# Kernel tuning notes

Measured on AMD Instinct MI355X. Metric: run time of the kernel, lower is better.

Reference implementation:

```python
import jax, jax.numpy as jnp
import numpy as np

D_MODEL = 1024
H = 16
D_K = D_MODEL // H
B, S = 2, 2048


def setup_inputs() -> dict:
    key = jax.random.key(0)
    ks = jax.random.split(key, 11)
    sc = 1.0 / np.sqrt(D_MODEL)
    inp = {
        "q": jax.random.normal(ks[0], (B, S, D_MODEL), jnp.float32),
        "k": jax.random.normal(ks[1], (B, S, D_MODEL), jnp.float32),
        "v": jax.random.normal(ks[2], (B, S, D_MODEL), jnp.float32),
        "mask": jnp.ones((1, 1, S, S), dtype=bool),
        # nn.Linear weights are [out, in]; y = x @ W.T + b
        "wq_w": jax.random.normal(ks[3], (D_MODEL, D_MODEL), jnp.float32) * sc,
        "wq_b": jnp.zeros((D_MODEL,), jnp.float32),
        "wk_w": jax.random.normal(ks[4], (D_MODEL, D_MODEL), jnp.float32) * sc,
        "wk_b": jnp.zeros((D_MODEL,), jnp.float32),
        "wv_w": jax.random.normal(ks[5], (D_MODEL, D_MODEL), jnp.float32) * sc,
        "wv_b": jnp.zeros((D_MODEL,), jnp.float32),
        "wo_w": jax.random.normal(ks[6], (D_MODEL, D_MODEL), jnp.float32) * sc,
        "wo_b": jnp.zeros((D_MODEL,), jnp.float32),
    }
    return inp


def _split_heads(x):
    b, s, _ = x.shape
    return x.reshape(b, s, H, D_K).transpose(0, 2, 1, 3)  # [B,H,S,Dk]


def reference(q, k, v, mask, wq_w, wq_b, wk_w, wk_b, wv_w, wv_b, wo_w, wo_b):
    # projections (nn.Linear: x @ W.T + b)
    qh = _split_heads(q @ wq_w.T + wq_b)
    kh = _split_heads(k @ wk_w.T + wk_b)
    vh = _split_heads(v @ wv_w.T + wv_b)
    # scaled dot-product attention with additive -1e9 masking
    scores = jnp.einsum("bhqd,bhkd->bhqk", qh, kh) / jnp.sqrt(jnp.float32(D_K))
    scores = jnp.where(mask, scores, jnp.float32(-1e9))
    attn = jax.nn.softmax(scores, axis=-1)  # dropout p=0.0 -> identity
    out = jnp.einsum("bhqk,bhkd->bhqd", attn, vh)
    out = out.transpose(0, 2, 1, 3).reshape(q.shape[0], q.shape[1], D_MODEL)
    return out @ wo_w.T + wo_b
```

## Files before the change

kernel.cpp:

```cpp
#include <hip/hip_runtime.h>
#include <hip/hip_bf16.h>


typedef unsigned short u16;
typedef unsigned int u32;
typedef short s16x4 __attribute__((ext_vector_type(4)));
typedef short s16x8 __attribute__((ext_vector_type(8)));
typedef float f32x4 __attribute__((ext_vector_type(4)));

#define NH 16

__device__ __forceinline__ u16 f2bf(float f) {
  u32 u = __builtin_bit_cast(u32, f);
  u32 r = (u + 0x7fffu + ((u >> 16) & 1u)) >> 16;
  return (u16)r;
}

__device__ __forceinline__ void stage16(const void* g, void* l) {
  __builtin_amdgcn_global_load_lds((const __attribute__((address_space(1))) void*)g,
                                   (__attribute__((address_space(3))) void*)l,
                                   16, 0, 0);
}

__global__ __launch_bounds__(256) void convert3(const float* __restrict__ a,
                                                const float* __restrict__ b,
                                                const float* __restrict__ c,
                                                u16* da, u16* db, u16* dc) {
  const float* s = blockIdx.y == 0 ? a : (blockIdx.y == 1 ? b : c);
  u16* d = blockIdx.y == 0 ? da : (blockIdx.y == 1 ? db : dc);
  int i = (blockIdx.x * 256 + threadIdx.x) * 4;
  f32x4 v = *(const f32x4*)(s + i);
  s16x4 o;
#pragma unroll
  for (int j = 0; j < 4; ++j) o[j] = (short)f2bf(v[j]);
  *(s16x4*)(d + i) = o;
}

__global__ __launch_bounds__(256) void convert4(const float* __restrict__ a,
                                                const float* __restrict__ b,
                                                const float* __restrict__ c,
                                                const float* __restrict__ e,
                                                u16* da, u16* db, u16* dc, u16* de) {
  const float* s = blockIdx.y == 0 ? a
                   : (blockIdx.y == 1 ? b : (blockIdx.y == 2 ? c : e));
  u16* d = blockIdx.y == 0 ? da : (blockIdx.y == 1 ? db : (blockIdx.y == 2 ? dc : de));
  int i = (blockIdx.x * 256 + threadIdx.x) * 4;
  f32x4 v = *(const f32x4*)(s + i);
  s16x4 o;
#pragma unroll
  for (int j = 0; j < 4; ++j) o[j] = (short)f2bf(v[j]);
  *(s16x4*)(d + i) = o;
}

#define GEMM_CORE(A_, W_)                                                      \
  const int tid = threadIdx.x;                                                 \
  const int lane = tid & 63;                                                   \
  const int wid = tid >> 6;                                                    \
  const int l16 = lane & 15, quad = lane >> 4;                                 \
  const int wm = (wid >> 1) * 64, wn = (wid & 1) * 64;                         \
  const int m0 = blockIdx.y * 128;                                             \
  const int n0 = blockIdx.x * 128;                                             \
  const int ra = tid >> 2;                                                     \
  const int c8 = (tid & 3) ^ (ra & 3);                                         \
  const u16* Abase = A_ + (size_t)(m0 + ra) * 1024 + c8 * 8;                   \
  const u16* A2 = Abase + (size_t)64 * 1024;                                   \
  const u16* Wbase = W_ + (size_t)(n0 + ra) * 1024 + c8 * 8;                   \
  const u16* W2 = Wbase + (size_t)64 * 1024;                                   \
  u16* ldsA = As + tid * 8;                                                    \
  u16* ldsB = Bs + tid * 8;                                                    \
  f32x4 acc[4][4];                                                             \
  _Pragma("unroll") for (int i = 0; i < 4; ++i)                                \
  _Pragma("unroll") for (int j = 0; j < 4; ++j)                                \
      acc[i][j] = (f32x4){0.f, 0.f, 0.f, 0.f};                                 \
  for (int k0 = 0; k0 < 1024; k0 += 32) {                                      \
    __syncthreads();                                                           \
    stage16(Abase + k0, ldsA);                                                 \
    stage16(A2 + k0, ldsA + 2048);                                             \
    stage16(Wbase + k0, ldsB);                                                 \
    stage16(W2 + k0, ldsB + 2048);                                             \
    __syncthreads();                                                           \
    s16x8 bfr[4];                                                              \
    _Pragma("unroll") for (int j = 0; j < 4; ++j) {                            \
      int row = wn + j * 16 + l16;                                             \
      bfr[j] = *(const s16x8*)&Bs[(row * 4 + (quad ^ (row & 3))) * 8];         \
    }                                                                          \
    _Pragma("unroll") for (int i = 0; i < 4; ++i) {                            \
      int row = wm + i * 16 + l16;                                             \
      s16x8 afr = *(const s16x8*)&As[(row * 4 + (quad ^ (row & 3))) * 8];      \
      _Pragma("unroll") for (int j = 0; j < 4; ++j)                            \
        acc[i][j] =                                                            \
            __builtin_amdgcn_mfma_f32_16x16x32_bf16(afr, bfr[j], acc[i][j],    \
                                                    0, 0, 0);                  \
    }                                                                          \
  }

__global__ __launch_bounds__(256, 3) void proj_kernel(
    const u16* __restrict__ q, const u16* __restrict__ k, const u16* __restrict__ v,
    const u16* __restrict__ wq, const u16* __restrict__ wk, const u16* __restrict__ wv,
    const float* __restrict__ bq, const float* __restrict__ bk,
    const float* __restrict__ bv,
    u16* __restrict__ Qh, u16* __restrict__ Kh, u16* __restrict__ VhT) {
  const int z = blockIdx.z;
  const u16* A_in = z == 0 ? q : (z == 1 ? k : v);
  const u16* W_in = z == 0 ? wq : (z == 1 ? wk : wv);
  const float* bias = z == 0 ? bq : (z == 1 ? bk : bv);

  __shared__ __align__(16) u16 As[128 * 32];
  __shared__ __align__(16) u16 Bs[128 * 32];

  GEMM_CORE(A_in, W_in)

  float bcol[4];
#pragma unroll
  for (int j = 0; j < 4; ++j) bcol[j] = bias[n0 + wn + j * 16 + l16];

  if (z < 2) {
    u16* out = (z == 0) ? Qh : Kh;
#pragma unroll
    for (int i = 0; i < 4; ++i) {
      int gm0 = m0 + wm + i * 16 + quad * 4;
      int b = gm0 >> 11, s = gm0 & 2047;
#pragma unroll
      for (int j = 0; j < 4; ++j) {
        int gn = n0 + wn + j * 16 + l16;
        int h = gn >> 6, dk = gn & 63;
        size_t base = ((size_t)(b * NH + h) * 2048 + s) * 64 + dk;
#pragma unroll
        for (int r = 0; r < 4; ++r)
          out[base + (size_t)r * 64] = f2bf(acc[i][j][r] + bcol[j]);
      }
    }
  } else {
#pragma unroll
    for (int i = 0; i < 4; ++i) {
      int gm0 = m0 + wm + i * 16 + quad * 4;
      int b = gm0 >> 11, s = gm0 & 2047;
#pragma unroll
      for (int j = 0; j < 4; ++j) {
        int gn = n0 + wn + j * 16 + l16;
        int h = gn >> 6, dk = gn & 63;
        size_t base = ((size_t)(b * NH + h) * 64 + dk) * 2048 + s;
        s16x4 pv;
#pragma unroll
        for (int r = 0; r < 4; ++r) pv[r] = (short)f2bf(acc[i][j][r] + bcol[j]);
        *(s16x4*)&VhT[base] = pv;
      }
    }
  }
}

__global__ __launch_bounds__(256, 3) void out_kernel(const u16* __restrict__ ctx,
                                                     const u16* __restrict__ wo,
                                                     const float* __restrict__ bo,
                                                     float* __restrict__ out) {
  __shared__ __align__(16) u16 As[128 * 32];
  __shared__ __align__(16) u16 Bs[128 * 32];

  GEMM_CORE(ctx, wo)

  float bcol[4];
#pragma unroll
  for (int j = 0; j < 4; ++j) bcol[j] = bo[n0 + wn + j * 16 + l16];

#pragma unroll
  for (int i = 0; i < 4; ++i) {
    int gm0 = m0 + wm + i * 16 + quad * 4;
#pragma unroll
    for (int j = 0; j < 4; ++j) {
      int gn = n0 + wn + j * 16 + l16;
#pragma unroll
      for (int r = 0; r < 4; ++r)
        out[(size_t)(gm0 + r) * 1024 + gn] = acc[i][j][r] + bcol[j];
    }
  }
}

__global__ __launch_bounds__(256, 2) void flash_kernel(const u16* __restrict__ Qh,
                                                       const u16* __restrict__ Kh,
                                                       const u16* __restrict__ VhT,
                                                       u16* __restrict__ ctx) {
  __shared__ __align__(16) u16 Qs[128 * 64];
  __shared__ __align__(16) u16 Ks[128 * 64];
  __shared__ __align__(16) u16 Vs[64 * 128];

  const int tid = threadIdx.x;
  const int lane = tid & 63;
  const int wid = tid >> 6;
  const int l16 = lane & 15, quad = lane >> 4;
  const int qt = blockIdx.x;
  const int bh = blockIdx.y;

  const u16* Qg = Qh + ((size_t)bh * 2048 + qt * 128) * 64;
  const u16* Kg = Kh + (size_t)bh * 2048 * 64;
  const u16* Vg = VhT + (size_t)bh * 64 * 2048;

  const int rq = tid >> 3;
  const int c8q = (tid & 7) ^ (rq & 7);
  const int rv = tid >> 4;
  const int c8v = (tid & 15) ^ (rv & 15);

#pragma unroll
  for (int i = 0; i < 4; ++i)
    stage16(Qg + (size_t)(rq + i * 32) * 64 + c8q * 8, Qs + tid * 8 + i * 2048);
  __syncthreads();

  s16x8 bq[2][2];
#pragma unroll
  for (int ct = 0; ct < 2; ++ct)
#pragma unroll
    for (int kk = 0; kk < 2; ++kk) {
      int row = wid * 32 + ct * 16 + l16;
      bq[ct][kk] = *(const s16x8*)&Qs[(row * 8 + ((kk * 4 + quad) ^ (row & 7))) * 8];
    }

  float m_[2] = {-1e30f, -1e30f};
  float l_[2] = {0.f, 0.f};
  f32x4 oacc[4][2];
#pragma unroll
  for (int d = 0; d < 4; ++d)
#pragma unroll
    for (int ct = 0; ct < 2; ++ct) oacc[d][ct] = (f32x4){0.f, 0.f, 0.f, 0.f};

  const float sc = 0.125f * 1.44269504088896340736f;

  for (int kt = 0; kt < 16; ++kt) {
    __syncthreads();
#pragma unroll
    for (int i = 0; i < 4; ++i)
      stage16(Kg + (size_t)(kt * 128 + rq + i * 32) * 64 + c8q * 8,
              Ks + tid * 8 + i * 2048);
#pragma unroll
    for (int i = 0; i < 4; ++i)
      stage16(Vg + (size_t)(rv + i * 16) * 2048 + kt * 128 + c8v * 8,
              Vs + tid * 8 + i * 2048);
    __syncthreads();

    f32x4 st[8][2];
#pragma unroll
    for (int rt = 0; rt < 8; ++rt) {
      int row = rt * 16 + l16;
      s16x8 ak0 = *(const s16x8*)&Ks[(row * 8 + (quad ^ (row & 7))) * 8];
      s16x8 ak1 = *(const s16x8*)&Ks[(row * 8 + ((4 + quad) ^ (row & 7))) * 8];
#pragma unroll
      for (int ct = 0; ct < 2; ++ct) {
        f32x4 t0 = __builtin_amdgcn_mfma_f32_16x16x32_bf16(
            ak0, bq[ct][0], (f32x4){0.f, 0.f, 0.f, 0.f}, 0, 0, 0);
        st[rt][ct] =
            __builtin_amdgcn_mfma_f32_16x16x32_bf16(ak1, bq[ct][1], t0, 0, 0, 0);
      }
    }

    float alpha[2];
#pragma unroll
    for (int ct = 0; ct < 2; ++ct) {
      float cm = -1e30f;
#pragma unroll
      for (int rt = 0; rt < 8; ++rt)
#pragma unroll
        for (int c = 0; c < 4; ++c) cm = fmaxf(cm, st[rt][ct][c]);
      cm = fmaxf(cm, __shfl_xor(cm, 16));
      cm = fmaxf(cm, __shfl_xor(cm, 32));
      float mnew = fmaxf(m_[ct], cm);
      alpha[ct] = __builtin_exp2f((m_[ct] - mnew) * sc);
      float neg = mnew * sc;
      float rs = 0.f;
#pragma unroll
      for (int rt = 0; rt < 8; ++rt)
#pragma unroll
        for (int c = 0; c < 4; ++c) {
          float p = __builtin_exp2f(st[rt][ct][c] * sc - neg);
          st[rt][ct][c] = p;
          rs += p;
        }
      rs += __shfl_xor(rs, 16);
      rs += __shfl_xor(rs, 32);
      l_[ct] = l_[ct] * alpha[ct] + rs;
      m_[ct] = mnew;
    }

#pragma unroll
    for (int d = 0; d < 4; ++d)
#pragma unroll
      for (int ct = 0; ct < 2; ++ct) oacc[d][ct] *= alpha[ct];

#pragma unroll
    for (int ts = 0; ts < 8; ++ts) {
      s16x4 bp[2];
#pragma unroll
      for (int ct = 0; ct < 2; ++ct) {
#pragma unroll
        for (int c = 0; c < 4; ++c) bp[ct][c] = (short)f2bf(st[ts][ct][c]);
      }
#pragma unroll
      for (int d = 0; d < 4; ++d) {
        int rowv = d * 16 + l16;
        const u16* vp = &Vs[(rowv * 16 + ((2 * ts + (quad >> 1)) ^ (rowv & 15))) * 8 +
                            (quad & 1) * 4];
        s16x4 av = *(const s16x4*)vp;
#pragma unroll
        for (int ct = 0; ct < 2; ++ct)
          oacc[d][ct] = __builtin_amdgcn_mfma_f32_16x16x16bf16_1k(av, bp[ct],
                                                                  oacc[d][ct], 0, 0, 0);
      }
    }
  }

  const int b = bh >> 4, h = bh & 15;
#pragma unroll
  for (int ct = 0; ct < 2; ++ct) {
    float inv = 1.f / l_[ct];
    int sg = qt * 128 + wid * 32 + ct * 16 + l16;
#pragma unroll
    for (int d = 0; d < 4; ++d) {
      int dk0 = d * 16 + quad * 4;
      size_t base = ((size_t)b * 2048 + sg) * 1024 + h * 64 + dk0;
      s16x4 pk;
#pragma unroll
      for (int r = 0; r < 4; ++r) pk[r] = (short)f2bf(oacc[d][ct][r] * inv);
      *(s16x4*)&ctx[base] = pk;
    }
  }
}

extern "C" void kernel_launch(void* const* d_in, const int* in_sizes, int n_in,
                              void* d_out, int out_size, void* d_ws, size_t ws_size,
                              hipStream_t stream) {
  const float* q = (const float*)d_in[0];
  const float* k = (const float*)d_in[1];
  const float* v = (const float*)d_in[2];
  const float* wq = (const float*)d_in[4];
  const float* bq = (const float*)d_in[5];
  const float* wk = (const float*)d_in[6];
  const float* bk = (const float*)d_in[7];
  const float* wv = (const float*)d_in[8];
  const float* bv = (const float*)d_in[9];
  const float* wo = (const float*)d_in[10];
  const float* bo = (const float*)d_in[11];

  const size_t M1 = 1024 * 1024;
  u16* ws = (u16*)d_ws;
  u16* qb = ws;
  u16* kb = ws + 4 * M1;
  u16* vb = ws + 8 * M1;
  u16* wqb = ws + 12 * M1;
  u16* wkb = ws + 13 * M1;
  u16* wvb = ws + 14 * M1;
  u16* wob = ws + 15 * M1;
  u16* Qh = ws + 16 * M1;
  u16* Kh = ws + 20 * M1;
  u16* VhT = ws + 24 * M1;
  u16* ctx = qb;

  convert3<<<dim3(4096, 3), 256, 0, stream>>>(q, k, v, qb, kb, vb);
  convert4<<<dim3(1024, 4), 256, 0, stream>>>(wq, wk, wv, wo, wqb, wkb, wvb, wob);
  proj_kernel<<<dim3(8, 32, 3), 256, 0, stream>>>(qb, kb, vb, wqb, wkb, wvb,
                                                  bq, bk, bv, Qh, Kh, VhT);
  flash_kernel<<<dim3(16, 32), 256, 0, stream>>>(Qh, Kh, VhT, ctx);
  out_kernel<<<dim3(8, 32), 256, 0, stream>>>(ctx, wob, bo, (float*)d_out);
}
```

Measured before the change: 273.6 us.

## Halve flash query tile, fold softmax scale into Q, merge convert kernels

The flash kernel now processes 64 query rows per block instead of 128, with one 16-row tile per wave, and sets launch bounds to 4 blocks per SM, doubling the grid. This cuts register pressure and raises occupancy, at the cost of reloading K/V twice as often. The softmax scale and log2e factor are folded into Q in the projection epilogue, removing per-element multiplies in the flash loop. Bf16 packing uses a cheaper round-half-up perm instead of round-to-nearest-even, and the two convert kernels are merged into one launch.

```diff
diff --git a/kernel.cpp b/kernel.cpp
--- a/kernel.cpp
+++ b/kernel.cpp
@@ -7,8 +7,10 @@
 typedef short s16x4 __attribute__((ext_vector_type(4)));
 typedef short s16x8 __attribute__((ext_vector_type(8)));
 typedef float f32x4 __attribute__((ext_vector_type(4)));
+typedef unsigned int u32x2 __attribute__((ext_vector_type(2)));
 
 #define NH 16
+#define SCQ 0.1803368801111204f
 
 __device__ __forceinline__ u16 f2bf(float f) {
   u32 u = __builtin_bit_cast(u32, f);
@@ -16,40 +18,41 @@
   return (u16)r;
 }
 
+__device__ __forceinline__ u32 pkbf(float a, float b) {
+  u32 ua = __builtin_bit_cast(u32, a) + 0x8000u;
+  u32 ub = __builtin_bit_cast(u32, b) + 0x8000u;
+  return __builtin_amdgcn_perm(ub, ua, 0x07060302);
+}
+
 __device__ __forceinline__ void stage16(const void* g, void* l) {
   __builtin_amdgcn_global_load_lds((const __attribute__((address_space(1))) void*)g,
                                    (__attribute__((address_space(3))) void*)l,
                                    16, 0, 0);
 }
 
-__global__ __launch_bounds__(256) void convert3(const float* __restrict__ a,
-                                                const float* __restrict__ b,
-                                                const float* __restrict__ c,
-                                                u16* da, u16* db, u16* dc) {
-  const float* s = blockIdx.y == 0 ? a : (blockIdx.y == 1 ? b : c);
-  u16* d = blockIdx.y == 0 ? da : (blockIdx.y == 1 ? db : dc);
-  int i = (blockIdx.x * 256 + threadIdx.x) * 4;
-  f32x4 v = *(const f32x4*)(s + i);
-  s16x4 o;
-#pragma unroll
-  for (int j = 0; j < 4; ++j) o[j] = (short)f2bf(v[j]);
-  *(s16x4*)(d + i) = o;
-}
-
-__global__ __launch_bounds__(256) void convert4(const float* __restrict__ a,
-                                                const float* __restrict__ b,
-                                                const float* __restrict__ c,
-                                                const float* __restrict__ e,
-                                                u16* da, u16* db, u16* dc, u16* de) {
-  const float* s = blockIdx.y == 0 ? a
-                   : (blockIdx.y == 1 ? b : (blockIdx.y == 2 ? c : e));
-  u16* d = blockIdx.y == 0 ? da : (blockIdx.y == 1 ? db : (blockIdx.y == 2 ? dc : de));
-  int i = (blockIdx.x * 256 + threadIdx.x) * 4;
-  f32x4 v = *(const f32x4*)(s + i);
-  s16x4 o;
-#pragma unroll
-  for (int j = 0; j < 4; ++j) o[j] = (short)f2bf(v[j]);
-  *(s16x4*)(d + i) = o;
+__global__ __launch_bounds__(256) void convert_all(
+    const float* __restrict__ q, const float* __restrict__ k,
+    const float* __restrict__ v, const float* __restrict__ wq,
+    const float* __restrict__ wk, const float* __restrict__ wv,
+    const float* __restrict__ wo, u16* qb, u16* kb, u16* vb, u16* wqb,
+    u16* wkb, u16* wvb, u16* wob) {
+  const int y = blockIdx.y;
+  const float* s;
+  u16* d;
+  int i;
+  if (y < 3) {
+    s = y == 0 ? q : (y == 1 ? k : v);
+    d = y == 0 ? qb : (y == 1 ? kb : vb);
+    i = (blockIdx.x * 256 + threadIdx.x) * 4;
+  } else {
+    int w = blockIdx.x >> 10, j = blockIdx.x & 1023;
+    s = w == 0 ? wq : (w == 1 ? wk : (w == 2 ? wv : wo));
+    d = w == 0 ? wqb : (w == 1 ? wkb : (w == 2 ? wvb : wob));
+    i = (j * 256 + threadIdx.x) * 4;
+  }
+  f32x4 val = *(const f32x4*)(s + i);
+  u32x2 o = {pkbf(val[0], val[1]), pkbf(val[2], val[3])};
+  *(u32x2*)(d + i) = o;
 }
 
 #define GEMM_CORE(A_, W_)                                                      \
@@ -115,6 +118,7 @@
   for (int j = 0; j < 4; ++j) bcol[j] = bias[n0 + wn + j * 16 + l16];
 
   if (z < 2) {
+    const float qs = (z == 0) ? SCQ : 1.0f;
     u16* out = (z == 0) ? Qh : Kh;
 #pragma unroll
     for (int i = 0; i < 4; ++i) {
@@ -127,7 +131,7 @@
         size_t base = ((size_t)(b * NH + h) * 2048 + s) * 64 + dk;
 #pragma unroll
         for (int r = 0; r < 4; ++r)
-          out[base + (size_t)r * 64] = f2bf(acc[i][j][r] + bcol[j]);
+          out[base + (size_t)r * 64] = f2bf((acc[i][j][r] + bcol[j]) * qs);
       }
     }
   } else {
@@ -175,11 +179,11 @@
   }
 }
 
-__global__ __launch_bounds__(256, 2) void flash_kernel(const u16* __restrict__ Qh,
+__global__ __launch_bounds__(256, 4) void flash_kernel(const u16* __restrict__ Qh,
                                                        const u16* __restrict__ Kh,
                                                        const u16* __restrict__ VhT,
                                                        u16* __restrict__ ctx) {
-  __shared__ __align__(16) u16 Qs[128 * 64];
+  __shared__ __align__(16) u16 Qs[64 * 64];
   __shared__ __align__(16) u16 Ks[128 * 64];
   __shared__ __align__(16) u16 Vs[64 * 128];
 
@@ -190,7 +194,7 @@
   const int qt = blockIdx.x;
   const int bh = blockIdx.y;
 
-  const u16* Qg = Qh + ((size_t)bh * 2048 + qt * 128) * 64;
+  const u16* Qg = Qh + ((size_t)bh * 2048 + qt * 64) * 64;
   const u16* Kg = Kh + (size_t)bh * 2048 * 64;
   const u16* Vg = VhT + (size_t)bh * 64 * 2048;
 
@@ -200,28 +204,21 @@
   const int c8v = (tid & 15) ^ (rv & 15);
 
 #pragma unroll
-  for (int i = 0; i < 4; ++i)
+  for (int i = 0; i < 2; ++i)
     stage16(Qg + (size_t)(rq + i * 32) * 64 + c8q * 8, Qs + tid * 8 + i * 2048);
   __syncthreads();
 
-  s16x8 bq[2][2];
-#pragma unroll
-  for (int ct = 0; ct < 2; ++ct)
-#pragma unroll
-    for (int kk = 0; kk < 2; ++kk) {
-      int row = wid * 32 + ct * 16 + l16;
-      bq[ct][kk] = *(const s16x8*)&Qs[(row * 8 + ((kk * 4 + quad) ^ (row & 7))) * 8];
-    }
-
-  float m_[2] = {-1e30f, -1e30f};
-  float l_[2] = {0.f, 0.f};
-  f32x4 oacc[4][2];
-#pragma unroll
-  for (int d = 0; d < 4; ++d)
-#pragma unroll
-    for (int ct = 0; ct < 2; ++ct) oacc[d][ct] = (f32x4){0.f, 0.f, 0.f, 0.f};
-
-  const float sc = 0.125f * 1.44269504088896340736f;
+  const int rowq = wid * 16 + l16;
+  s16x8 bq[2];
+#pragma unroll
+  for (int kk = 0; kk < 2; ++kk)
+    bq[kk] = *(const s16x8*)&Qs[(rowq * 8 + ((kk * 4 + quad) ^ (rowq & 7))) * 8];
+
+  float m_ = -1e30f;
+  float l_ = 0.f;
+  f32x4 oacc[4];
+#pragma unroll
+  for (int d = 0; d < 4; ++d) oacc[d] = (f32x4){0.f, 0.f, 0.f, 0.f};
 
   for (int kt = 0; kt < 16; ++kt) {
     __syncthreads();
@@ -235,90 +232,68 @@
               Vs + tid * 8 + i * 2048);
     __syncthreads();
 
-    f32x4 st[8][2];
+    f32x4 st[8];
 #pragma unroll
     for (int rt = 0; rt < 8; ++rt) {
       int row = rt * 16 + l16;
       s16x8 ak0 = *(const s16x8*)&Ks[(row * 8 + (quad ^ (row & 7))) * 8];
       s16x8 ak1 = *(const s16x8*)&Ks[(row * 8 + ((4 + quad) ^ (row & 7))) * 8];
-#pragma unroll
-      for (int ct = 0; ct < 2; ++ct) {
-        f32x4 t0 = __builtin_amdgcn_mfma_f32_16x16x32_bf16(
-            ak0, bq[ct][0], (f32x4){0.f, 0.f, 0.f, 0.f}, 0, 0, 0);
-        st[rt][ct] =
-            __builtin_amdgcn_mfma_f32_16x16x32_bf16(ak1, bq[ct][1], t0, 0, 0, 0);
+      f32x4 t0 = __builtin_amdgcn_mfma_f32_16x16x32_bf16(
+          ak0, bq[0], (f32x4){0.f, 0.f, 0.f, 0.f}, 0, 0, 0);
+      st[rt] = __builtin_amdgcn_mfma_f32_16x16x32_bf16(ak1, bq[1], t0, 0, 0, 0);
+    }
+
+    float cm = -1e30f;
+#pragma unroll
+    for (int rt = 0; rt < 8; ++rt)
+#pragma unroll
+      for (int c = 0; c < 4; ++c) cm = fmaxf(cm, st[rt][c]);
+    cm = fmaxf(cm, __shfl_xor(cm, 16));
+    cm = fmaxf(cm, __shfl_xor(cm, 32));
+    float mnew = fmaxf(m_, cm);
+    float alpha = __builtin_exp2f(m_ - mnew);
+    float rs = 0.f;
+#pragma unroll
+    for (int rt = 0; rt < 8; ++rt)
+#pragma unroll
+      for (int c = 0; c < 4; ++c) {
+        float p = __builtin_exp2f(st[rt][c] - mnew);
+        st[rt][c] = p;
+        rs += p;
       }
-    }
-
-    float alpha[2];
-#pragma unroll
-    for (int ct = 0; ct < 2; ++ct) {
-      float cm = -1e30f;
-#pragma unroll
-      for (int rt = 0; rt < 8; ++rt)
-#pragma unroll
-        for (int c = 0; c < 4; ++c) cm = fmaxf(cm, st[rt][ct][c]);
-      cm = fmaxf(cm, __shfl_xor(cm, 16));
-      cm = fmaxf(cm, __shfl_xor(cm, 32));
-      float mnew = fmaxf(m_[ct], cm);
-      alpha[ct] = __builtin_exp2f((m_[ct] - mnew) * sc);
-      float neg = mnew * sc;
-      float rs = 0.f;
-#pragma unroll
-      for (int rt = 0; rt < 8; ++rt)
-#pragma unroll
-        for (int c = 0; c < 4; ++c) {
-          float p = __builtin_exp2f(st[rt][ct][c] * sc - neg);
-          st[rt][ct][c] = p;
-          rs += p;
-        }
-      rs += __shfl_xor(rs, 16);
-      rs += __shfl_xor(rs, 32);
-      l_[ct] = l_[ct] * alpha[ct] + rs;
-      m_[ct] = mnew;
-    }
-
-#pragma unroll
-    for (int d = 0; d < 4; ++d)
-#pragma unroll
-      for (int ct = 0; ct < 2; ++ct) oacc[d][ct] *= alpha[ct];
+    rs += __shfl_xor(rs, 16);
+    rs += __shfl_xor(rs, 32);
+    l_ = l_ * alpha + rs;
+    m_ = mnew;
+
+#pragma unroll
+    for (int d = 0; d < 4; ++d) oacc[d] *= alpha;
 
 #pragma unroll
     for (int ts = 0; ts < 8; ++ts) {
-      s16x4 bp[2];
-#pragma unroll
-      for (int ct = 0; ct < 2; ++ct) {
-#pragma unroll
-        for (int c = 0; c < 4; ++c) bp[ct][c] = (short)f2bf(st[ts][ct][c]);
-      }
+      u32x2 bpu = {pkbf(st[ts][0], st[ts][1]), pkbf(st[ts][2], st[ts][3])};
+      s16x4 bp = __builtin_bit_cast(s16x4, bpu);
 #pragma unroll
       for (int d = 0; d < 4; ++d) {
         int rowv = d * 16 + l16;
         const u16* vp = &Vs[(rowv * 16 + ((2 * ts + (quad >> 1)) ^ (rowv & 15))) * 8 +
                             (quad & 1) * 4];
         s16x4 av = *(const s16x4*)vp;
-#pragma unroll
-        for (int ct = 0; ct < 2; ++ct)
-          oacc[d][ct] = __builtin_amdgcn_mfma_f32_16x16x16bf16_1k(av, bp[ct],
-                                                                  oacc[d][ct], 0, 0, 0);
+        oacc[d] = __builtin_amdgcn_mfma_f32_16x16x16bf16_1k(av, bp, oacc[d], 0, 0, 0);
       }
     }
   }
 
   const int b = bh >> 4, h = bh & 15;
-#pragma unroll
-  for (int ct = 0; ct < 2; ++ct) {
-    float inv = 1.f / l_[ct];
-    int sg = qt * 128 + wid * 32 + ct * 16 + l16;
-#pragma unroll
-    for (int d = 0; d < 4; ++d) {
-      int dk0 = d * 16 + quad * 4;
-      size_t base = ((size_t)b * 2048 + sg) * 1024 + h * 64 + dk0;
-      s16x4 pk;
-#pragma unroll
-      for (int r = 0; r < 4; ++r) pk[r] = (short)f2bf(oacc[d][ct][r] * inv);
-      *(s16x4*)&ctx[base] = pk;
-    }
+  const float inv = 1.f / l_;
+  const int sg = qt * 64 + rowq;
+#pragma unroll
+  for (int d = 0; d < 4; ++d) {
+    int dk0 = d * 16 + quad * 4;
+    size_t base = ((size_t)b * 2048 + sg) * 1024 + h * 64 + dk0;
+    u32x2 pk = {pkbf(oacc[d][0] * inv, oacc[d][1] * inv),
+                pkbf(oacc[d][2] * inv, oacc[d][3] * inv)};
+    *(u32x2*)&ctx[base] = pk;
   }
 }
 
@@ -351,10 +326,10 @@
   u16* VhT = ws + 24 * M1;
   u16* ctx = qb;
 
-  convert3<<<dim3(4096, 3), 256, 0, stream>>>(q, k, v, qb, kb, vb);
-  convert4<<<dim3(1024, 4), 256, 0, stream>>>(wq, wk, wv, wo, wqb, wkb, wvb, wob);
+  convert_all<<<dim3(4096, 4), 256, 0, stream>>>(q, k, v, wq, wk, wv, wo, qb, kb,
+                                                 vb, wqb, wkb, wvb, wob);
   proj_kernel<<<dim3(8, 32, 3), 256, 0, stream>>>(qb, kb, vb, wqb, wkb, wvb,
                                                   bq, bk, bv, Qh, Kh, VhT);
-  flash_kernel<<<dim3(16, 32), 256, 0, stream>>>(Qh, Kh, VhT, ctx);
+  flash_kernel<<<dim3(32, 32), 256, 0, stream>>>(Qh, Kh, VhT, ctx);
   out_kernel<<<dim3(8, 32), 256, 0, stream>>>(ctx, wob, bo, (float*)d_out);
 }
```

After: 264.8 us. -3.2%, faster.
